# Kernel optimization log

Measured on AMD Instinct MI355X. Metric: run time of the kernel, lower is better.

The kernel has to match this reference:

```python
import jax, jax.numpy as jnp
import numpy as np

SEQ, B, IN, H = 512, 64, 1024, 1024


def setup_inputs() -> dict:
    key = jax.random.key(0)
    ks = jax.random.split(key, 7)
    s = 1.0 / np.sqrt(H)
    return {
        "inp": jax.random.normal(ks[0], (SEQ, B, IN), dtype=jnp.float32),
        "h0": jax.random.normal(ks[1], (1, B, H), dtype=jnp.float32),
        "c0": jax.random.normal(ks[2], (1, B, H), dtype=jnp.float32),
        "W_ih": jax.random.uniform(ks[3], (4 * H, IN), jnp.float32, -s, s),
        "W_hh": jax.random.uniform(ks[4], (4 * H, H), jnp.float32, -s, s),
        "b_ih": jax.random.uniform(ks[5], (4 * H,), jnp.float32, -s, s),
        "b_hh": jax.random.uniform(ks[6], (4 * H,), jnp.float32, -s, s),
    }


def _lstm_scan(x_bsi, h, c, W_ih, W_hh, b_ih, b_hh):
    # Precompute input projections for all timesteps in one big GEMM: (B,S,4H)
    x_proj = jnp.einsum("bsi,gi->bsg", x_bsi, W_ih) + (b_ih + b_hh)

    def step(carry, xp):
        h, c = carry  # (B,H) each; xp: (B,4H)
        gates = xp + h @ W_hh.T
        i, f, g, o = jnp.split(gates, 4, axis=-1)
        c = jax.nn.sigmoid(f) * c + jax.nn.sigmoid(i) * jnp.tanh(g)
        h = jax.nn.sigmoid(o) * jnp.tanh(c)
        return (h, c), h

    (h, c), ys = jax.lax.scan(step, (h, c), jnp.swapaxes(x_proj, 0, 1))
    return ys, h, c  # ys: (S,B,H) with ys[t] = h_t


def reference(inp, h0, c0, W_ih, W_hh, b_ih, b_hh):
    seq_len, batch, _ = inp.shape
    # Faithful to torch: .view reshapes (memory reinterpretation), NOT transpose
    x = inp.reshape(batch, seq_len, -1)          # (B,S,I)
    h = h0.reshape(batch, -1)                    # (B,H)
    c = c0.reshape(batch, -1)                    # (B,H)
    ys, h, c = _lstm_scan(x, h, c, W_ih, W_hh, b_ih, b_hh)
    # torch builds output (B,S,H) with output[:, t] = h_t, then views to (S,B,H)
    output = jnp.swapaxes(ys, 0, 1).reshape(seq_len, batch, -1)
    return output, (h.reshape(-1, batch, H), c.reshape(-1, batch, H))
```

## Files before the change

kernel.cpp:

```cpp
#include <hip/hip_runtime.h>
#include <cstdint>


typedef __bf16 bf16x8 __attribute__((ext_vector_type(8)));
typedef __bf16 bf16x4 __attribute__((ext_vector_type(4)));
typedef float  floatx4 __attribute__((ext_vector_type(4)));

#define SEQ   512
#define BATCH 64
#define HID   1024
#define GATES 4096
#define TC    128

__device__ __forceinline__ float fast_sigm(float x) {
  return 1.0f / (1.0f + __expf(-x));
}
__device__ __forceinline__ float fast_tanh(float x) {
  x = fminf(15.0f, fmaxf(-15.0f, x));
  float e = __expf(2.0f * x);
  return (e - 1.0f) / (e + 1.0f);
}

__global__ void cast_f32_to_bf16_x4(const float* __restrict__ src,
                                    __bf16* __restrict__ dst, int n4) {
  int i = blockIdx.x * blockDim.x + threadIdx.x;
  if (i < n4) {
    float4 v = reinterpret_cast<const float4*>(src)[i];
    bf16x4 o;
    o[0] = (__bf16)v.x; o[1] = (__bf16)v.y; o[2] = (__bf16)v.z; o[3] = (__bf16)v.w;
    reinterpret_cast<bf16x4*>(dst)[i] = o;
  }
}

__global__ void bias_sum(const float* __restrict__ a, const float* __restrict__ b,
                         float* __restrict__ o) {
  int i = blockIdx.x * blockDim.x + threadIdx.x;
  if (i < GATES) o[i] = a[i] + b[i];
}

__global__ __launch_bounds__(256) void gemm_xproj(
    const __bf16* __restrict__ X,
    const __bf16* __restrict__ W,
    const float*  __restrict__ bias,
    float*        __restrict__ XP,
    int t0) {
  __shared__ __bf16 As[128][40];
  __shared__ __bf16 Bs[128][40];

  const int tid  = threadIdx.x;
  const int lane = tid & 63;
  const int w    = tid >> 6;
  const int wm   = w >> 1, wn = w & 1;
  const int mt   = blockIdx.x;
  const int n0   = blockIdx.y * 128;
  const long arow0 = (long)mt * 512 + t0;

  floatx4 acc[4][4] = {};

  for (int k0 = 0; k0 < 1024; k0 += 32) {
    __syncthreads();
#pragma unroll
    for (int r = 0; r < 2; ++r) {
      int c = tid + 256 * r;
      int row = c >> 2, c8 = c & 3;
      *reinterpret_cast<uint4*>(&As[row][c8 * 8]) =
          *reinterpret_cast<const uint4*>(&X[(arow0 + row) * 1024 + k0 + c8 * 8]);
      *reinterpret_cast<uint4*>(&Bs[row][c8 * 8]) =
          *reinterpret_cast<const uint4*>(&W[(long)(n0 + row) * 1024 + k0 + c8 * 8]);
    }
    __syncthreads();

    bf16x8 a[4], b[4];
#pragma unroll
    for (int i = 0; i < 4; ++i)
      a[i] = *reinterpret_cast<const __shared__ bf16x8*>(
          &As[wm * 64 + i * 16 + (lane & 15)][(lane >> 4) * 8]);
#pragma unroll
    for (int j = 0; j < 4; ++j)
      b[j] = *reinterpret_cast<const __shared__ bf16x8*>(
          &Bs[wn * 64 + j * 16 + (lane & 15)][(lane >> 4) * 8]);
#pragma unroll
    for (int i = 0; i < 4; ++i)
#pragma unroll
      for (int j = 0; j < 4; ++j)
        acc[i][j] = __builtin_amdgcn_mfma_f32_16x16x32_bf16(a[i], b[j], acc[i][j], 0, 0, 0);
  }

#pragma unroll
  for (int i = 0; i < 4; ++i) {
    int mloc = wm * 64 + i * 16 + (lane >> 4) * 4;
#pragma unroll
    for (int j = 0; j < 4; ++j) {
      int n = n0 + wn * 64 + j * 16 + (lane & 15);
      float bn = bias[n];
#pragma unroll
      for (int r = 0; r < 4; ++r)
        XP[(long)(mt * 128 + mloc + r) * 4096 + n] = acc[i][j][r] + bn;
    }
  }
}

__global__ __launch_bounds__(256) void lstm_step(
    const __bf16* __restrict__ hin,
    __bf16*       __restrict__ hout,
    float*        __restrict__ cst,
    const __bf16* __restrict__ Whh,
    const float*  __restrict__ xp,
    float*        __restrict__ out,
    int t) {
  __shared__ __bf16 Hs[16][1032];
  __shared__ __bf16 Bs[64][264];
  __shared__ float  Gs[4][16][17];

  const int tid  = threadIdx.x;
  const int lane = tid & 63;
  const int w    = tid >> 6;
  const int j0   = blockIdx.x * 16;
  const int b0   = blockIdx.y * 16;

#pragma unroll
  for (int r = 0; r < 8; ++r) {
    int c = tid + 256 * r;
    int row = c >> 7, c8 = c & 127;
    *reinterpret_cast<uint4*>(&Hs[row][c8 * 8]) =
        *reinterpret_cast<const uint4*>(&hin[(b0 + row) * 1024 + c8 * 8]);
  }

  floatx4 acc = {};
  for (int kc = 0; kc < 4; ++kc) {
    __syncthreads();
#pragma unroll
    for (int r = 0; r < 8; ++r) {
      int c = tid + 256 * r;
      int rb = c >> 5, c8 = c & 31;
      int grow = (rb >> 4) * 1024 + j0 + (rb & 15);
      *reinterpret_cast<uint4*>(&Bs[rb][c8 * 8]) =
          *reinterpret_cast<const uint4*>(&Whh[(long)grow * 1024 + kc * 256 + c8 * 8]);
    }
    __syncthreads();
#pragma unroll
    for (int q = 0; q < 8; ++q) {
      bf16x8 a = *reinterpret_cast<const __shared__ bf16x8*>(
          &Hs[lane & 15][kc * 256 + q * 32 + (lane >> 4) * 8]);
      bf16x8 b = *reinterpret_cast<const __shared__ bf16x8*>(
          &Bs[w * 16 + (lane & 15)][q * 32 + (lane >> 4) * 8]);
      acc = __builtin_amdgcn_mfma_f32_16x16x32_bf16(a, b, acc, 0, 0, 0);
    }
  }

#pragma unroll
  for (int r = 0; r < 4; ++r)
    Gs[w][(lane >> 4) * 4 + r][lane & 15] = acc[r];
  __syncthreads();

  int bb = tid >> 4, jj = tid & 15;
  int b = b0 + bb, j = j0 + jj;
  int tt = t & (TC - 1);
  const float* xr = &xp[((long)b * TC + tt) * 4096 + j];
  float gi = Gs[0][bb][jj] + xr[0];
  float gf = Gs[1][bb][jj] + xr[1024];
  float gg = Gs[2][bb][jj] + xr[2048];
  float go = Gs[3][bb][jj] + xr[3072];
  float c_old = cst[b * 1024 + j];
  float c_new = fast_sigm(gf) * c_old + fast_sigm(gi) * fast_tanh(gg);
  float h_new = fast_sigm(go) * fast_tanh(c_new);
  cst[b * 1024 + j]  = c_new;
  hout[b * 1024 + j] = (__bf16)h_new;
  out[(long)b * (SEQ * HID) + (long)t * HID + j] = h_new;
  if (t == SEQ - 1) {
    out[(long)SEQ * BATCH * HID + b * HID + j] = h_new;
    out[(long)SEQ * BATCH * HID + BATCH * HID + b * HID + j] = c_new;
  }
}

extern "C" void kernel_launch(void* const* d_in, const int* in_sizes, int n_in,
                              void* d_out, int out_size, void* d_ws, size_t ws_size,
                              hipStream_t stream) {
  const float* inp = (const float*)d_in[0];
  const float* h0  = (const float*)d_in[1];
  const float* c0  = (const float*)d_in[2];
  const float* Wih = (const float*)d_in[3];
  const float* Whh = (const float*)d_in[4];
  const float* bih = (const float*)d_in[5];
  const float* bhh = (const float*)d_in[6];
  float* out = (float*)d_out;
  char* ws = (char*)d_ws;

  size_t off = 0;
  __bf16* Wih_b = (__bf16*)(ws + off); off += (size_t)GATES * HID * 2;
  __bf16* Whh_b = (__bf16*)(ws + off); off += (size_t)GATES * HID * 2;
  __bf16* x_b   = (__bf16*)(ws + off); off += (size_t)SEQ * BATCH * HID * 2;
  float*  xp    = (float*)(ws + off);  off += (size_t)BATCH * TC * GATES * 4;
  float*  bias  = (float*)(ws + off);  off += (size_t)GATES * 4;
  float*  cst   = (float*)(ws + off);  off += (size_t)BATCH * HID * 4;
  __bf16* hb0   = (__bf16*)(ws + off); off += (size_t)BATCH * HID * 2;
  __bf16* hb1   = (__bf16*)(ws + off); off += (size_t)BATCH * HID * 2;
  if (ws_size < off) return;

  int n4;
  n4 = GATES * HID / 4;
  cast_f32_to_bf16_x4<<<(n4 + 255) / 256, 256, 0, stream>>>(Wih, Wih_b, n4);
  cast_f32_to_bf16_x4<<<(n4 + 255) / 256, 256, 0, stream>>>(Whh, Whh_b, n4);
  n4 = SEQ * BATCH * HID / 4;
  cast_f32_to_bf16_x4<<<(n4 + 255) / 256, 256, 0, stream>>>(inp, x_b, n4);
  n4 = BATCH * HID / 4;
  cast_f32_to_bf16_x4<<<(n4 + 255) / 256, 256, 0, stream>>>(h0, hb0, n4);
  bias_sum<<<GATES / 256, 256, 0, stream>>>(bih, bhh, bias);
  hipMemcpyAsync(cst, c0, (size_t)BATCH * HID * 4, hipMemcpyDeviceToDevice, stream);

  __bf16* hbuf[2] = {hb0, hb1};
  for (int chunk = 0; chunk < SEQ / TC; ++chunk) {
    int t0 = chunk * TC;
    gemm_xproj<<<dim3(BATCH, GATES / 128), 256, 0, stream>>>(x_b, Wih_b, bias, xp, t0);
    for (int tt = 0; tt < TC; ++tt) {
      int t = t0 + tt;
      lstm_step<<<dim3(HID / 16, BATCH / 16), 256, 0, stream>>>(
          hbuf[t & 1], hbuf[(t + 1) & 1], cst, Whh_b, xp, out, t);
    }
  }
}
```

Measured before the change: 3.767 ms.

## Replace per-timestep launches with persistent recurrent kernel using grid barriers

Per-step LSTM kernel launches are replaced by one persistent kernel per chunk of 128 timesteps. Each block keeps its slice of W_hh in registers and the cell state in a register. Blocks within a batch tile synchronise each step through a global atomic counter barrier. This removes launch overhead and the repeated reloading of W_hh, but assumes all 256 blocks are co-resident, and the per-step barrier spin adds latency and a deadlock risk.

```diff
diff --git a/kernel.cpp b/kernel.cpp
--- a/kernel.cpp
+++ b/kernel.cpp
@@ -73,11 +73,11 @@
     bf16x8 a[4], b[4];
 #pragma unroll
     for (int i = 0; i < 4; ++i)
-      a[i] = *reinterpret_cast<const __shared__ bf16x8*>(
+      a[i] = *reinterpret_cast<const bf16x8*>(
           &As[wm * 64 + i * 16 + (lane & 15)][(lane >> 4) * 8]);
 #pragma unroll
     for (int j = 0; j < 4; ++j)
-      b[j] = *reinterpret_cast<const __shared__ bf16x8*>(
+      b[j] = *reinterpret_cast<const bf16x8*>(
           &Bs[wn * 64 + j * 16 + (lane & 15)][(lane >> 4) * 8]);
 #pragma unroll
     for (int i = 0; i < 4; ++i)
@@ -100,77 +100,110 @@
   }
 }
 
-__global__ __launch_bounds__(256) void lstm_step(
-    const __bf16* __restrict__ hin,
-    __bf16*       __restrict__ hout,
-    float*        __restrict__ cst,
+__global__ __launch_bounds__(256) void lstm_recur(
     const __bf16* __restrict__ Whh,
     const float*  __restrict__ xp,
-    float*        __restrict__ out,
-    int t) {
+    __bf16* hb0, __bf16* hb1,
+    float*  __restrict__ cst,
+    float*  __restrict__ out,
+    unsigned* bar,
+    int t0) {
   __shared__ __bf16 Hs[16][1032];
-  __shared__ __bf16 Bs[64][264];
-  __shared__ float  Gs[4][16][17];
+  __shared__ float  Gred[4][4][16][17];
 
   const int tid  = threadIdx.x;
   const int lane = tid & 63;
   const int w    = tid >> 6;
-  const int j0   = blockIdx.x * 16;
-  const int b0   = blockIdx.y * 16;
-
-#pragma unroll
-  for (int r = 0; r < 8; ++r) {
-    int c = tid + 256 * r;
-    int row = c >> 7, c8 = c & 127;
-    *reinterpret_cast<uint4*>(&Hs[row][c8 * 8]) =
-        *reinterpret_cast<const uint4*>(&hin[(b0 + row) * 1024 + c8 * 8]);
-  }
-
-  floatx4 acc = {};
-  for (int kc = 0; kc < 4; ++kc) {
-    __syncthreads();
-#pragma unroll
-    for (int r = 0; r < 8; ++r) {
-      int c = tid + 256 * r;
-      int rb = c >> 5, c8 = c & 31;
-      int grow = (rb >> 4) * 1024 + j0 + (rb & 15);
-      *reinterpret_cast<uint4*>(&Bs[rb][c8 * 8]) =
-          *reinterpret_cast<const uint4*>(&Whh[(long)grow * 1024 + kc * 256 + c8 * 8]);
-    }
-    __syncthreads();
-#pragma unroll
-    for (int q = 0; q < 8; ++q) {
-      bf16x8 a = *reinterpret_cast<const __shared__ bf16x8*>(
-          &Hs[lane & 15][kc * 256 + q * 32 + (lane >> 4) * 8]);
-      bf16x8 b = *reinterpret_cast<const __shared__ bf16x8*>(
-          &Bs[w * 16 + (lane & 15)][q * 32 + (lane >> 4) * 8]);
-      acc = __builtin_amdgcn_mfma_f32_16x16x32_bf16(a, b, acc, 0, 0, 0);
-    }
-  }
-
-#pragma unroll
-  for (int r = 0; r < 4; ++r)
-    Gs[w][(lane >> 4) * 4 + r][lane & 15] = acc[r];
-  __syncthreads();
-
-  int bb = tid >> 4, jj = tid & 15;
-  int b = b0 + bb, j = j0 + jj;
-  int tt = t & (TC - 1);
-  const float* xr = &xp[((long)b * TC + tt) * 4096 + j];
-  float gi = Gs[0][bb][jj] + xr[0];
-  float gf = Gs[1][bb][jj] + xr[1024];
-  float gg = Gs[2][bb][jj] + xr[2048];
-  float go = Gs[3][bb][jj] + xr[3072];
-  float c_old = cst[b * 1024 + j];
-  float c_new = fast_sigm(gf) * c_old + fast_sigm(gi) * fast_tanh(gg);
-  float h_new = fast_sigm(go) * fast_tanh(c_new);
-  cst[b * 1024 + j]  = c_new;
-  hout[b * 1024 + j] = (__bf16)h_new;
-  out[(long)b * (SEQ * HID) + (long)t * HID + j] = h_new;
-  if (t == SEQ - 1) {
-    out[(long)SEQ * BATCH * HID + b * HID + j] = h_new;
-    out[(long)SEQ * BATCH * HID + BATCH * HID + b * HID + j] = c_new;
-  }
+  const int jt   = blockIdx.x;
+  const int bt   = blockIdx.y;
+  const int b0   = bt * 16;
+
+  bf16x8 breg[4][8];
+  {
+    const int n = lane & 15, u = lane >> 4;
+#pragma unroll
+    for (int g = 0; g < 4; ++g)
+#pragma unroll
+      for (int q = 0; q < 8; ++q)
+        breg[g][q] = *reinterpret_cast<const bf16x8*>(
+            &Whh[(long)(g * 1024 + jt * 16 + n) * 1024 + w * 256 + q * 32 + u * 8]);
+  }
+
+  const int bth = tid >> 4;
+  const int jl  = tid & 15;
+  const int j   = jt * 16 + jl;
+  float c_reg = cst[(b0 + bth) * 1024 + j];
+
+  unsigned* mybar = bar + bt * 64;
+
+  for (int tt = 0; tt < TC; ++tt) {
+    const int t = t0 + tt;
+    const __bf16* hc = (t & 1) ? hb1 : hb0;
+    __bf16*       hn = (t & 1) ? hb0 : hb1;
+
+    const float* xr = &xp[((long)(b0 + bth) * TC + tt) * 4096 + j];
+    float xq0 = xr[0], xq1 = xr[1024], xq2 = xr[2048], xq3 = xr[3072];
+
+    uint4 hv[8];
+    {
+      const __bf16* src = &hc[(b0 + bth) * 1024 + jl * 8];
+#pragma unroll
+      for (int k = 0; k < 8; ++k)
+        hv[k] = *reinterpret_cast<const uint4*>(&src[k * 128]);
+    }
+#pragma unroll
+    for (int k = 0; k < 8; ++k)
+      *reinterpret_cast<uint4*>(&Hs[bth][jl * 8 + k * 128]) = hv[k];
+    __syncthreads();
+
+    floatx4 acc[4] = {};
+    {
+      const int m = lane & 15, u = lane >> 4;
+#pragma unroll
+      for (int q = 0; q < 8; ++q) {
+        bf16x8 a = *reinterpret_cast<const bf16x8*>(&Hs[m][w * 256 + q * 32 + u * 8]);
+#pragma unroll
+        for (int g = 0; g < 4; ++g)
+          acc[g] = __builtin_amdgcn_mfma_f32_16x16x32_bf16(a, breg[g][q], acc[g], 0, 0, 0);
+      }
+    }
+    {
+      const int n = lane & 15, u = lane >> 4;
+#pragma unroll
+      for (int g = 0; g < 4; ++g)
+#pragma unroll
+        for (int r = 0; r < 4; ++r)
+          Gred[w][g][u * 4 + r][n] = acc[g][r];
+    }
+    __syncthreads();
+
+    float gi = Gred[0][0][bth][jl] + Gred[1][0][bth][jl] + Gred[2][0][bth][jl] + Gred[3][0][bth][jl] + xq0;
+    float gf = Gred[0][1][bth][jl] + Gred[1][1][bth][jl] + Gred[2][1][bth][jl] + Gred[3][1][bth][jl] + xq1;
+    float gg = Gred[0][2][bth][jl] + Gred[1][2][bth][jl] + Gred[2][2][bth][jl] + Gred[3][2][bth][jl] + xq2;
+    float go = Gred[0][3][bth][jl] + Gred[1][3][bth][jl] + Gred[2][3][bth][jl] + Gred[3][3][bth][jl] + xq3;
+
+    float c_new = fast_sigm(gf) * c_reg + fast_sigm(gi) * fast_tanh(gg);
+    float h_new = fast_sigm(go) * fast_tanh(c_new);
+    c_reg = c_new;
+    hn[(b0 + bth) * 1024 + j] = (__bf16)h_new;
+    out[(long)(b0 + bth) * (SEQ * HID) + (long)t * HID + j] = h_new;
+    if (t == SEQ - 1) {
+      out[(long)SEQ * BATCH * HID + (b0 + bth) * HID + j] = h_new;
+      out[(long)SEQ * BATCH * HID + BATCH * HID + (b0 + bth) * HID + j] = c_new;
+    }
+
+    __syncthreads();
+    if (tid == 0) {
+      __hip_atomic_fetch_add(mybar, 1u, __ATOMIC_RELEASE, __HIP_MEMORY_SCOPE_AGENT);
+      const unsigned target = 64u * (unsigned)(t + 1);
+      while (__hip_atomic_load(mybar, __ATOMIC_RELAXED, __HIP_MEMORY_SCOPE_AGENT) < target)
+        __builtin_amdgcn_s_sleep(1);
+      (void)__hip_atomic_load(mybar, __ATOMIC_ACQUIRE, __HIP_MEMORY_SCOPE_AGENT);
+    }
+    __syncthreads();
+  }
+
+  cst[(b0 + bth) * 1024 + j] = c_reg;
 }
 
 extern "C" void kernel_launch(void* const* d_in, const int* in_sizes, int n_in,
@@ -195,6 +228,7 @@
   float*  cst   = (float*)(ws + off);  off += (size_t)BATCH * HID * 4;
   __bf16* hb0   = (__bf16*)(ws + off); off += (size_t)BATCH * HID * 2;
   __bf16* hb1   = (__bf16*)(ws + off); off += (size_t)BATCH * HID * 2;
+  unsigned* bar = (unsigned*)(ws + off); off += 4 * 64 * sizeof(unsigned);
   if (ws_size < off) return;
 
   int n4;
@@ -207,15 +241,11 @@
   cast_f32_to_bf16_x4<<<(n4 + 255) / 256, 256, 0, stream>>>(h0, hb0, n4);
   bias_sum<<<GATES / 256, 256, 0, stream>>>(bih, bhh, bias);
   hipMemcpyAsync(cst, c0, (size_t)BATCH * HID * 4, hipMemcpyDeviceToDevice, stream);
-
-  __bf16* hbuf[2] = {hb0, hb1};
+  hipMemsetAsync(bar, 0, 4 * 64 * sizeof(unsigned), stream);
+
   for (int chunk = 0; chunk < SEQ / TC; ++chunk) {
     int t0 = chunk * TC;
     gemm_xproj<<<dim3(BATCH, GATES / 128), 256, 0, stream>>>(x_b, Wih_b, bias, xp, t0);
-    for (int tt = 0; tt < TC; ++tt) {
-      int t = t0 + tt;
-      lstm_step<<<dim3(HID / 16, BATCH / 16), 256, 0, stream>>>(
-          hbuf[t & 1], hbuf[(t + 1) & 1], cst, Whh_b, xp, out, t);
-    }
-  }
-}
+    lstm_recur<<<dim3(64, 4), 256, 0, stream>>>(Whh_b, xp, hb0, hb1, cst, out, bar, t0);
+  }
+}
```

After: 6.101 ms. 62.0% more time.
